# Performance work log

Hardware: AMD Instinct MI355X
Metric: run time of the kernel (lower is better)

Reference implementation:

```python
import jax, jax.numpy as jnp
import numpy as np

N, E, D, L = 50000, 800000, 128, 2
EPS = 1e-10


def mobius_add(x, y, c):
    # c: shape [1], broadcasts against [N,1]
    xy = jnp.sum(x * y, axis=-1, keepdims=True)
    x2 = jnp.sum(x * x, axis=-1, keepdims=True)
    y2 = jnp.sum(y * y, axis=-1, keepdims=True)
    num = (1 + 2 * c * xy + c * y2) * x + (1 - c * x2) * y
    den = 1 + 2 * c * xy + (c ** 2) * x2 * y2
    return num / den


def log_map(x, y, c):
    ym = mobius_add(-x, y, c)
    n = jnp.maximum(jnp.linalg.norm(ym, axis=-1, keepdims=True), EPS)
    sc = jnp.sqrt(c)
    return (2.0 / sc) * jnp.arctanh(sc * n) * ym / n


def exp_map(x, v, c):
    n = jnp.maximum(jnp.linalg.norm(v, axis=-1, keepdims=True), EPS)
    sc = jnp.sqrt(c)
    second = jnp.tanh(sc * n / 2.0) * v / (sc * n)
    return mobius_add(x, second, c)


def l2norm(x):
    return x / jnp.maximum(jnp.linalg.norm(x, axis=-1, keepdims=True), 1e-12)


def mean_agg(h, src, dst, n_nodes):
    # copy_u + mean reduce: mean of h[src] grouped by dst; zero-degree -> 0
    msum = jax.ops.segment_sum(h[src], dst, num_segments=n_nodes)
    deg = jax.ops.segment_sum(jnp.ones((src.shape[0], 1), h.dtype), dst, num_segments=n_nodes)
    return msum / jnp.maximum(deg, 1.0)


def setup_inputs() -> dict:
    key = jax.random.key(0)
    ks = jax.random.split(key, 12)
    scale = 1.0 / np.sqrt(D)
    return {
        "src": jax.random.randint(ks[0], (E,), 0, N, dtype=jnp.int32),
        "dst": jax.random.randint(ks[1], (E,), 0, N, dtype=jnp.int32),
        "e_emb": jax.random.normal(ks[2], (N, D), dtype=jnp.float32),
        "b_emb": 0.01 * jax.random.normal(ks[3], (N, D), dtype=jnp.float32),  # inside Poincare ball
        "s_emb": jax.random.normal(ks[4], (N, D), dtype=jnp.float32),
        "e_W": scale * jax.random.normal(ks[5], (L, D, D), dtype=jnp.float32),
        "e_b": jnp.zeros((L, D), dtype=jnp.float32),
        "b_W": scale * jax.random.normal(ks[6], (L, D, D), dtype=jnp.float32),
        "b_b": jnp.zeros((L, D), dtype=jnp.float32),
        "s_W": scale * jax.random.normal(ks[7], (L, D, D), dtype=jnp.float32),
        "s_b": jnp.zeros((L, D), dtype=jnp.float32),
        "b_curvature": jnp.ones((1,), dtype=jnp.float32),
        "s_curvature": jnp.ones((1,), dtype=jnp.float32),
    }


def reference(src, dst, e_emb, b_emb, s_emb, e_W, e_b, b_W, b_b, s_W, s_b, b_curvature, s_curvature):
    n = e_emb.shape[0]
    origin = jnp.zeros((1, b_emb.shape[-1]), dtype=b_emb.dtype)
    for l in range(L):
        # Euclidean: transform -> mean aggregate -> LeakyReLU(0.2)
        h = e_emb @ e_W[l].T + e_b[l]
        e_emb = mean_agg(h, src, dst, n)
        e_emb = jnp.where(e_emb > 0, e_emb, 0.2 * e_emb)
        # Hyperbolic: log map to tangent -> transform -> mean aggregate -> exp map
        tangent = log_map(origin, b_emb, b_curvature)
        hb = tangent @ b_W[l].T + b_b[l]
        neigh_b = mean_agg(hb, src, dst, n)
        b_emb = exp_map(origin, neigh_b, b_curvature)
        # Spherical: normalize -> transform -> normalize -> mean aggregate -> normalize
        hs = l2norm(l2norm(s_emb) @ s_W[l].T + s_b[l])
        s_emb = l2norm(mean_agg(hs, src, dst, n))
    return (e_emb, b_emb, s_emb)
```

## Files before the change

### kernel.cpp

```cpp
#include <hip/hip_runtime.h>
#include <math.h>

#define DD 128
typedef unsigned int   u32;
typedef unsigned short u16;
typedef short bf16x8 __attribute__((ext_vector_type(8)));
typedef float f32x4  __attribute__((ext_vector_type(4)));

__device__ __forceinline__ float lo2f(u32 p){ return __uint_as_float(p << 16); }
__device__ __forceinline__ float hi2f(u32 p){ return __uint_as_float(p & 0xFFFF0000u); }
__device__ __forceinline__ u16 f2bf(float f){
    u32 u = __float_as_uint(f);
    return (u16)((u + 0x7fffu + ((u >> 16) & 1u)) >> 16);
}

__global__ void k_hist(const int* __restrict__ dst, int* __restrict__ deg, int E){
    int i = blockIdx.x*256 + threadIdx.x;
    if (i < E) atomicAdd(&deg[dst[i]], 1);
}

__global__ void k_chunksum(const int* __restrict__ deg, int* __restrict__ csum,
                           float* __restrict__ invdeg, int n){
    __shared__ int sdata[256];
    int t = threadIdx.x;
    int i0 = blockIdx.x*512 + t*2;
    int a = (i0     < n) ? deg[i0]   : 0;
    int b = (i0 + 1 < n) ? deg[i0+1] : 0;
    if (i0     < n) invdeg[i0]   = 1.0f / (float)max(a, 1);
    if (i0 + 1 < n) invdeg[i0+1] = 1.0f / (float)max(b, 1);
    sdata[t] = a + b; __syncthreads();
    for (int off = 128; off > 0; off >>= 1){
        if (t < off) sdata[t] += sdata[t+off];
        __syncthreads();
    }
    if (t == 0) csum[blockIdx.x] = sdata[0];
}

__global__ void k_scanchunks(int* __restrict__ csum, int nchunks, int* __restrict__ row_ptr, int n){
    if (threadIdx.x == 0){
        int acc = 0;
        for (int i = 0; i < nchunks; i++){ int v = csum[i]; csum[i] = acc; acc += v; }
        row_ptr[n] = acc;
    }
}

__global__ void k_scanwithin(const int* __restrict__ deg, const int* __restrict__ csum,
                             int* __restrict__ row_ptr, int n){
    __shared__ int s[256];
    int t = threadIdx.x;
    int i0 = blockIdx.x*512 + t*2;
    int a = (i0     < n) ? deg[i0]   : 0;
    int b = (i0 + 1 < n) ? deg[i0+1] : 0;
    int tsum = a + b;
    s[t] = tsum; __syncthreads();
    for (int off = 1; off < 256; off <<= 1){
        int v = (t >= off) ? s[t-off] : 0;
        __syncthreads();
        s[t] += v;
        __syncthreads();
    }
    int excl = s[t] - tsum + csum[blockIdx.x];
    if (i0     < n) row_ptr[i0]   = excl;
    if (i0 + 1 < n) row_ptr[i0+1] = excl + a;
}

__global__ void k_fill(const int* __restrict__ src, const int* __restrict__ dst,
                       const int* __restrict__ row_ptr, int* __restrict__ cursor,
                       int* __restrict__ sorted_src, int E){
    int i = blockIdx.x*256 + threadIdx.x;
    if (i < E){
        int d = dst[i];
        int p = atomicAdd(&cursor[d], 1);
        sorted_src[row_ptr[d] + p] = src[i];
    }
}

__global__ void k_w2b(const float* __restrict__ in, u16* __restrict__ out, int n){
    int i = blockIdx.x*256 + threadIdx.x;
    if (i < n) out[i] = f2bf(in[i]);
}

template<int PRE, int POST>
__global__ __launch_bounds__(256, 4)
void k_gemm_mfma(const float* __restrict__ X, const u16* __restrict__ Wb,
                 const float* __restrict__ bias, u16* __restrict__ Y, int n_rows,
                 const float* __restrict__ cptr){
    int t = threadIdx.x;
    int wave = t >> 6, lane = t & 63;
    int q = lane >> 4, m = lane & 15;
    int rowbase = blockIdx.x*64 + wave*16;
    int gr = min(rowbase + m, n_rows - 1);

    float4 xv[8];
    const float4* xp = (const float4*)(X + (size_t)gr*DD);
    #pragma unroll
    for (int c = 0; c < 4; c++){
        xv[2*c]   = xp[c*8 + q*2];
        xv[2*c+1] = xp[c*8 + q*2 + 1];
    }

    float scale = 1.0f;
    if (PRE != 0){
        float ss = 0.f;
        #pragma unroll
        for (int i = 0; i < 8; i++)
            ss += xv[i].x*xv[i].x + xv[i].y*xv[i].y + xv[i].z*xv[i].z + xv[i].w*xv[i].w;
        ss += __shfl_xor(ss, 16, 64);
        ss += __shfl_xor(ss, 32, 64);
        float nrm = sqrtf(ss);
        if (PRE == 1){
            float c  = cptr[0];
            c = (c > 0.f && c < 1e30f) ? c : 1.0f;
            float sc = sqrtf(c);
            float n2 = fmaxf(nrm, 1e-10f);
            float a  = fminf(sc*n2, 0.99999994f);
            scale = (2.0f/sc) * atanhf(a) / n2;
        } else {
            scale = 1.0f / fmaxf(nrm, 1e-12f);
        }
    }

    bf16x8 af[4];
    #pragma unroll
    for (int c = 0; c < 4; c++){
        const float* xf = (const float*)&xv[2*c];
        #pragma unroll
        for (int j = 0; j < 8; j++) af[c][j] = (short)f2bf(xf[j]*scale);
    }

    f32x4 acc[8];
    #pragma unroll
    for (int tl = 0; tl < 8; tl++) acc[tl] = (f32x4){0.f,0.f,0.f,0.f};

    const u16* wb = Wb + (size_t)m*DD + q*8;
    #pragma unroll
    for (int c = 0; c < 4; c++){
        #pragma unroll
        for (int tl = 0; tl < 8; tl++){
            bf16x8 bfr = *(const bf16x8*)(wb + (size_t)tl*16*DD + c*32);
            acc[tl] = __builtin_amdgcn_mfma_f32_16x16x32_bf16(af[c], bfr, acc[tl], 0, 0, 0);
        }
    }

    #pragma unroll
    for (int tl = 0; tl < 8; tl++){
        float bv = bias[tl*16 + m];
        #pragma unroll
        for (int r = 0; r < 4; r++) acc[tl][r] += bv;
    }
    if (POST == 1){
        float ssr[4] = {0.f,0.f,0.f,0.f};
        #pragma unroll
        for (int tl = 0; tl < 8; tl++)
            #pragma unroll
            for (int r = 0; r < 4; r++) ssr[r] += acc[tl][r]*acc[tl][r];
        #pragma unroll
        for (int r = 0; r < 4; r++){
            float s = ssr[r];
            s += __shfl_xor(s, 1, 64);
            s += __shfl_xor(s, 2, 64);
            s += __shfl_xor(s, 4, 64);
            s += __shfl_xor(s, 8, 64);
            float sc = 1.0f / fmaxf(sqrtf(s), 1e-12f);
            #pragma unroll
            for (int tl = 0; tl < 8; tl++) acc[tl][r] *= sc;
        }
    }
    #pragma unroll
    for (int r = 0; r < 4; r++){
        int grow = rowbase + q*4 + r;
        if (grow < n_rows){
            #pragma unroll
            for (int tl = 0; tl < 8; tl++)
                Y[(size_t)grow*DD + tl*16 + m] = f2bf(acc[tl][r]);
        }
    }
}

template<int MODE>
__global__ void k_agg(const u32* __restrict__ h,
                      const int* __restrict__ row_ptr, const int* __restrict__ sorted_src,
                      const float* __restrict__ invdeg,
                      float* __restrict__ outbuf, int n_rows, const float* __restrict__ cptr){
    int wid = (blockIdx.x*256 + threadIdx.x) >> 6;
    if (wid >= n_rows) return;
    int lane = threadIdx.x & 63;
    int beg = row_ptr[wid], end = row_ptr[wid+1];
    float ax = 0.f, ay = 0.f;
    for (int j0 = beg; j0 < end; j0 += 64){
        int cnt = min(64, end - j0);
        int my = (j0 + lane < end) ? sorted_src[j0 + lane] : 0;
        int k = 0;
        for (; k + 8 <= cnt; k += 8){
            u32 p0 = h[(size_t)__shfl(my, k+0, 64)*64 + lane];
            u32 p1 = h[(size_t)__shfl(my, k+1, 64)*64 + lane];
            u32 p2 = h[(size_t)__shfl(my, k+2, 64)*64 + lane];
            u32 p3 = h[(size_t)__shfl(my, k+3, 64)*64 + lane];
            u32 p4 = h[(size_t)__shfl(my, k+4, 64)*64 + lane];
            u32 p5 = h[(size_t)__shfl(my, k+5, 64)*64 + lane];
            u32 p6 = h[(size_t)__shfl(my, k+6, 64)*64 + lane];
            u32 p7 = h[(size_t)__shfl(my, k+7, 64)*64 + lane];
            ax += lo2f(p0); ay += hi2f(p0);
            ax += lo2f(p1); ay += hi2f(p1);
            ax += lo2f(p2); ay += hi2f(p2);
            ax += lo2f(p3); ay += hi2f(p3);
            ax += lo2f(p4); ay += hi2f(p4);
            ax += lo2f(p5); ay += hi2f(p5);
            ax += lo2f(p6); ay += hi2f(p6);
            ax += lo2f(p7); ay += hi2f(p7);
        }
        for (; k < cnt; k++){
            u32 p = h[(size_t)__shfl(my, k, 64)*64 + lane];
            ax += lo2f(p); ay += hi2f(p);
        }
    }
    float inv = invdeg[wid];
    ax *= inv; ay *= inv;
    float ox, oy;
    if (MODE == 0){
        ox = ax > 0.f ? ax : 0.2f*ax;
        oy = ay > 0.f ? ay : 0.2f*ay;
    } else {
        float ss = ax*ax + ay*ay;
        #pragma unroll
        for (int m = 32; m > 0; m >>= 1) ss += __shfl_xor(ss, m, 64);
        float nrm = sqrtf(ss);
        float scale;
        if (MODE == 1){
            float c  = cptr[0];
            c = (c > 0.f && c < 1e30f) ? c : 1.0f;
            float sc = sqrtf(c);
            float n2 = fmaxf(nrm, 1e-10f);
            scale = tanhf(sc*n2*0.5f) / (sc*n2);
        } else {
            scale = 1.0f / fmaxf(nrm, 1e-12f);
        }
        ox = ax*scale; oy = ay*scale;
    }
    *(float2*)(outbuf + (size_t)wid*DD + lane*2) = make_float2(ox, oy);
}

extern "C" void kernel_launch(void* const* d_in, const int* in_sizes, int n_in,
                              void* d_out, int out_size, void* d_ws, size_t ws_size,
                              hipStream_t stream){
    const int*   src = (const int*)d_in[0];
    const int*   dst = (const int*)d_in[1];
    const float* emb_in[3] = {(const float*)d_in[2], (const float*)d_in[3], (const float*)d_in[4]};
    const float* W_in[3]   = {(const float*)d_in[5], (const float*)d_in[7], (const float*)d_in[9]};
    const float* b_in[3]   = {(const float*)d_in[6], (const float*)d_in[8], (const float*)d_in[10]};
    const float* b_c       = (const float*)d_in[11];

    const int E  = in_sizes[0];
    const int ND = in_sizes[2];
    const int N  = ND / DD;
    const int Lnum = in_sizes[5] / (DD*DD);
    const int nw = Lnum*DD*DD;
    const int nchunks = (N + 511) / 512;

    char* w = (char*)d_ws;
    auto alloc = [&](size_t bytes)->char*{
        char* p = w; w += (bytes + 255) & ~(size_t)255; return p;
    };
    u32*   h         = (u32*)  alloc((size_t)ND*2);
    u16*   Wb[3];
    for (int i = 0; i < 3; i++) Wb[i] = (u16*)alloc((size_t)nw*2);
    float* invdeg    = (float*)alloc((size_t)N*4);
    int*   deg       = (int*)  alloc((size_t)N*4);
    int*   row_ptr   = (int*)  alloc((size_t)(N+1)*4);
    int*   cursor    = (int*)  alloc((size_t)N*4);
    int*   csum      = (int*)  alloc((size_t)nchunks*4);
    int*   sorted_src= (int*)  alloc((size_t)E*4);
    (void)ws_size; (void)n_in; (void)out_size;

    float* out_e = (float*)d_out;
    float* out_b = out_e + ND;
    float* out_s = out_e + 2*ND;

    hipMemsetAsync(deg,    0, (size_t)N*4, stream);
    hipMemsetAsync(cursor, 0, (size_t)N*4, stream);

    const int TB = 256;
    for (int i = 0; i < 3; i++)
        k_w2b<<<(nw+TB-1)/TB, TB, 0, stream>>>(W_in[i], Wb[i], nw);

    k_hist<<<(E+TB-1)/TB, TB, 0, stream>>>(dst, deg, E);
    k_chunksum<<<nchunks, 256, 0, stream>>>(deg, csum, invdeg, N);
    k_scanchunks<<<1, 64, 0, stream>>>(csum, nchunks, row_ptr, N);
    k_scanwithin<<<nchunks, 256, 0, stream>>>(deg, csum, row_ptr, N);
    k_fill<<<(E+TB-1)/TB, TB, 0, stream>>>(src, dst, row_ptr, cursor, sorted_src, E);

    const int rowblocks  = (N + 3) / 4;
    const int gemmblocks = (N + 63) / 64;

    const float* se = emb_in[0];
    const float* sb = emb_in[1];
    const float* ss = emb_in[2];

    for (int l = 0; l < Lnum; l++){
        k_gemm_mfma<0,0><<<gemmblocks, 256, 0, stream>>>(se, Wb[0] + (size_t)l*DD*DD,
                                                         b_in[0] + (size_t)l*DD, (u16*)h, N, b_c);
        k_agg<0><<<rowblocks, 256, 0, stream>>>(h, row_ptr, sorted_src, invdeg, out_e, N, b_c);
        se = out_e;
        k_gemm_mfma<1,0><<<gemmblocks, 256, 0, stream>>>(sb, Wb[1] + (size_t)l*DD*DD,
                                                         b_in[1] + (size_t)l*DD, (u16*)h, N, b_c);
        k_agg<1><<<rowblocks, 256, 0, stream>>>(h, row_ptr, sorted_src, invdeg, out_b, N, b_c);
        sb = out_b;
        k_gemm_mfma<2,1><<<gemmblocks, 256, 0, stream>>>(ss, Wb[2] + (size_t)l*DD*DD,
                                                         b_in[2] + (size_t)l*DD, (u16*)h, N, b_c);
        k_agg<2><<<rowblocks, 256, 0, stream>>>(h, row_ptr, sorted_src, invdeg, out_s, N, b_c);
        ss = out_s;
    }
}
```

Measured before the change: 580.1 us.

## Fuse three branch GEMMs and aggregations into single kernels with vectorized gathers

Batches the Euclidean, hyperbolic and spherical GEMMs into one launch using a grid y-dimension, and fuses the three mean aggregations into one kernel that reads the neighbour list once and gathers 16-byte chunks for all three feature buffers. Each wave now handles four edges in parallel with lane groups and reduces across groups via shuffles. The chunk scan is parallelized, and the fill kernel writes cursor positions directly, which removes one memset and the row_ptr lookup. This needs three bf16 intermediate buffers instead of one and increases register pressure in the aggregation kernel.

```diff
diff --git a/kernel.cpp b/kernel.cpp
--- a/kernel.cpp
+++ b/kernel.cpp
@@ -36,16 +36,37 @@
     if (t == 0) csum[blockIdx.x] = sdata[0];
 }
 
-__global__ void k_scanchunks(int* __restrict__ csum, int nchunks, int* __restrict__ row_ptr, int n){
-    if (threadIdx.x == 0){
-        int acc = 0;
-        for (int i = 0; i < nchunks; i++){ int v = csum[i]; csum[i] = acc; acc += v; }
-        row_ptr[n] = acc;
-    }
+__global__ void k_scanchunks(int* __restrict__ csum, int nchunks,
+                             int* __restrict__ row_ptr, int n){
+    __shared__ int s[256];
+    __shared__ int carry_sh;
+    int t = threadIdx.x;
+    if (t == 0) carry_sh = 0;
+    __syncthreads();
+    for (int base = 0; base < nchunks; base += 256){
+        int i = base + t;
+        int v = (i < nchunks) ? csum[i] : 0;
+        s[t] = v;
+        __syncthreads();
+        for (int off = 1; off < 256; off <<= 1){
+            int u = (t >= off) ? s[t-off] : 0;
+            __syncthreads();
+            s[t] += u;
+            __syncthreads();
+        }
+        int carry = carry_sh;
+        int excl  = carry + s[t] - v;
+        if (i < nchunks) csum[i] = excl;
+        int tot = s[255];
+        __syncthreads();
+        if (t == 0) carry_sh = carry + tot;
+        __syncthreads();
+    }
+    if (t == 0) row_ptr[n] = carry_sh;
 }
 
 __global__ void k_scanwithin(const int* __restrict__ deg, const int* __restrict__ csum,
-                             int* __restrict__ row_ptr, int n){
+                             int* __restrict__ row_ptr, int* __restrict__ cursor, int n){
     __shared__ int s[256];
     int t = threadIdx.x;
     int i0 = blockIdx.x*512 + t*2;
@@ -60,31 +81,34 @@
         __syncthreads();
     }
     int excl = s[t] - tsum + csum[blockIdx.x];
-    if (i0     < n) row_ptr[i0]   = excl;
-    if (i0 + 1 < n) row_ptr[i0+1] = excl + a;
+    if (i0     < n){ row_ptr[i0]   = excl;     cursor[i0]   = excl;     }
+    if (i0 + 1 < n){ row_ptr[i0+1] = excl + a; cursor[i0+1] = excl + a; }
 }
 
 __global__ void k_fill(const int* __restrict__ src, const int* __restrict__ dst,
-                       const int* __restrict__ row_ptr, int* __restrict__ cursor,
-                       int* __restrict__ sorted_src, int E){
+                       int* __restrict__ cursor, int* __restrict__ sorted_src, int E){
     int i = blockIdx.x*256 + threadIdx.x;
     if (i < E){
-        int d = dst[i];
-        int p = atomicAdd(&cursor[d], 1);
-        sorted_src[row_ptr[d] + p] = src[i];
-    }
-}
-
-__global__ void k_w2b(const float* __restrict__ in, u16* __restrict__ out, int n){
+        int p = atomicAdd(&cursor[dst[i]], 1);
+        sorted_src[p] = src[i];
+    }
+}
+
+__global__ void k_w2b3(const float* __restrict__ w0, const float* __restrict__ w1,
+                       const float* __restrict__ w2,
+                       u16* __restrict__ o0, u16* __restrict__ o1, u16* __restrict__ o2,
+                       int nw){
     int i = blockIdx.x*256 + threadIdx.x;
-    if (i < n) out[i] = f2bf(in[i]);
+    if (i >= nw) return;
+    const float* s = (blockIdx.y == 0) ? w0 : (blockIdx.y == 1) ? w1 : w2;
+    u16*         o = (blockIdx.y == 0) ? o0 : (blockIdx.y == 1) ? o1 : o2;
+    o[i] = f2bf(s[i]);
 }
 
 template<int PRE, int POST>
-__global__ __launch_bounds__(256, 4)
-void k_gemm_mfma(const float* __restrict__ X, const u16* __restrict__ Wb,
-                 const float* __restrict__ bias, u16* __restrict__ Y, int n_rows,
-                 const float* __restrict__ cptr){
+__device__ __forceinline__ void gemm_body(const float* __restrict__ X, const u16* __restrict__ Wb,
+                                          const float* __restrict__ bias, u16* __restrict__ Y,
+                                          int n_rows, const float* __restrict__ cptr){
     int t = threadIdx.x;
     int wave = t >> 6, lane = t & 63;
     int q = lane >> 4, m = lane & 15;
@@ -177,67 +201,103 @@
     }
 }
 
-template<int MODE>
-__global__ void k_agg(const u32* __restrict__ h,
-                      const int* __restrict__ row_ptr, const int* __restrict__ sorted_src,
-                      const float* __restrict__ invdeg,
-                      float* __restrict__ outbuf, int n_rows, const float* __restrict__ cptr){
+__global__ __launch_bounds__(256, 4)
+void k_gemm3(const float* __restrict__ Xe, const float* __restrict__ Xb, const float* __restrict__ Xs,
+             const u16* __restrict__ We, const u16* __restrict__ Wh, const u16* __restrict__ Ws,
+             const float* __restrict__ be, const float* __restrict__ bb, const float* __restrict__ bs,
+             u16* __restrict__ Ye, u16* __restrict__ Yb, u16* __restrict__ Ys,
+             int n_rows, const float* __restrict__ cptr){
+    if (blockIdx.y == 0)      gemm_body<0,0>(Xe, We, be, Ye, n_rows, cptr);
+    else if (blockIdx.y == 1) gemm_body<1,0>(Xb, Wh, bb, Yb, n_rows, cptr);
+    else                      gemm_body<2,1>(Xs, Ws, bs, Ys, n_rows, cptr);
+}
+
+__device__ __forceinline__ void acc8(float* a, uint4 p){
+    a[0] += lo2f(p.x); a[1] += hi2f(p.x);
+    a[2] += lo2f(p.y); a[3] += hi2f(p.y);
+    a[4] += lo2f(p.z); a[5] += hi2f(p.z);
+    a[6] += lo2f(p.w); a[7] += hi2f(p.w);
+}
+
+__global__ __launch_bounds__(256)
+void k_agg3(const u32* __restrict__ he, const u32* __restrict__ hb, const u32* __restrict__ hs,
+            const int* __restrict__ row_ptr, const int* __restrict__ sorted_src,
+            const float* __restrict__ invdeg,
+            float* __restrict__ out_e, float* __restrict__ out_b, float* __restrict__ out_s,
+            int n_rows, const float* __restrict__ cptr){
     int wid = (blockIdx.x*256 + threadIdx.x) >> 6;
     if (wid >= n_rows) return;
     int lane = threadIdx.x & 63;
+    int g = lane >> 4, c = lane & 15;
     int beg = row_ptr[wid], end = row_ptr[wid+1];
-    float ax = 0.f, ay = 0.f;
-    for (int j0 = beg; j0 < end; j0 += 64){
-        int cnt = min(64, end - j0);
-        int my = (j0 + lane < end) ? sorted_src[j0 + lane] : 0;
-        int k = 0;
-        for (; k + 8 <= cnt; k += 8){
-            u32 p0 = h[(size_t)__shfl(my, k+0, 64)*64 + lane];
-            u32 p1 = h[(size_t)__shfl(my, k+1, 64)*64 + lane];
-            u32 p2 = h[(size_t)__shfl(my, k+2, 64)*64 + lane];
-            u32 p3 = h[(size_t)__shfl(my, k+3, 64)*64 + lane];
-            u32 p4 = h[(size_t)__shfl(my, k+4, 64)*64 + lane];
-            u32 p5 = h[(size_t)__shfl(my, k+5, 64)*64 + lane];
-            u32 p6 = h[(size_t)__shfl(my, k+6, 64)*64 + lane];
-            u32 p7 = h[(size_t)__shfl(my, k+7, 64)*64 + lane];
-            ax += lo2f(p0); ay += hi2f(p0);
-            ax += lo2f(p1); ay += hi2f(p1);
-            ax += lo2f(p2); ay += hi2f(p2);
-            ax += lo2f(p3); ay += hi2f(p3);
-            ax += lo2f(p4); ay += hi2f(p4);
-            ax += lo2f(p5); ay += hi2f(p5);
-            ax += lo2f(p6); ay += hi2f(p6);
-            ax += lo2f(p7); ay += hi2f(p7);
-        }
-        for (; k < cnt; k++){
-            u32 p = h[(size_t)__shfl(my, k, 64)*64 + lane];
-            ax += lo2f(p); ay += hi2f(p);
-        }
+    int coff = c*4;
+
+    float ae[8], ab[8], as_[8];
+    #pragma unroll
+    for (int i = 0; i < 8; i++){ ae[i] = 0.f; ab[i] = 0.f; as_[i] = 0.f; }
+
+    int p = beg + g;
+    for (; p + 4 < end; p += 8){
+        size_t o0 = (size_t)sorted_src[p]  *64 + coff;
+        size_t o1 = (size_t)sorted_src[p+4]*64 + coff;
+        uint4 e0 = *(const uint4*)(he + o0);
+        uint4 b0 = *(const uint4*)(hb + o0);
+        uint4 s0 = *(const uint4*)(hs + o0);
+        uint4 e1 = *(const uint4*)(he + o1);
+        uint4 b1 = *(const uint4*)(hb + o1);
+        uint4 s1 = *(const uint4*)(hs + o1);
+        acc8(ae, e0); acc8(ab, b0); acc8(as_, s0);
+        acc8(ae, e1); acc8(ab, b1); acc8(as_, s1);
+    }
+    if (p < end){
+        size_t o0 = (size_t)sorted_src[p]*64 + coff;
+        uint4 e0 = *(const uint4*)(he + o0);
+        uint4 b0 = *(const uint4*)(hb + o0);
+        uint4 s0 = *(const uint4*)(hs + o0);
+        acc8(ae, e0); acc8(ab, b0); acc8(as_, s0);
+    }
+
+    #pragma unroll
+    for (int i = 0; i < 8; i++){
+        ae[i]  += __shfl_xor(ae[i],  16, 64); ae[i]  += __shfl_xor(ae[i],  32, 64);
+        ab[i]  += __shfl_xor(ab[i],  16, 64); ab[i]  += __shfl_xor(ab[i],  32, 64);
+        as_[i] += __shfl_xor(as_[i], 16, 64); as_[i] += __shfl_xor(as_[i], 32, 64);
     }
     float inv = invdeg[wid];
-    ax *= inv; ay *= inv;
-    float ox, oy;
-    if (MODE == 0){
-        ox = ax > 0.f ? ax : 0.2f*ax;
-        oy = ay > 0.f ? ay : 0.2f*ay;
-    } else {
-        float ss = ax*ax + ay*ay;
-        #pragma unroll
-        for (int m = 32; m > 0; m >>= 1) ss += __shfl_xor(ss, m, 64);
-        float nrm = sqrtf(ss);
-        float scale;
-        if (MODE == 1){
-            float c  = cptr[0];
-            c = (c > 0.f && c < 1e30f) ? c : 1.0f;
-            float sc = sqrtf(c);
-            float n2 = fmaxf(nrm, 1e-10f);
-            scale = tanhf(sc*n2*0.5f) / (sc*n2);
-        } else {
-            scale = 1.0f / fmaxf(nrm, 1e-12f);
-        }
-        ox = ax*scale; oy = ay*scale;
-    }
-    *(float2*)(outbuf + (size_t)wid*DD + lane*2) = make_float2(ox, oy);
+    #pragma unroll
+    for (int i = 0; i < 8; i++){ ae[i] *= inv; ab[i] *= inv; as_[i] *= inv; }
+
+    float ssb = 0.f, sss = 0.f;
+    #pragma unroll
+    for (int i = 0; i < 8; i++){ ssb += ab[i]*ab[i]; sss += as_[i]*as_[i]; }
+    #pragma unroll
+    for (int msk = 1; msk < 16; msk <<= 1){
+        ssb += __shfl_xor(ssb, msk, 64);
+        sss += __shfl_xor(sss, msk, 64);
+    }
+
+    if (g == 0){
+        float o[8];
+        #pragma unroll
+        for (int i = 0; i < 8; i++) o[i] = ae[i] > 0.f ? ae[i] : 0.2f*ae[i];
+        float4* dstp = (float4*)(out_e + (size_t)wid*DD + c*8);
+        dstp[0] = make_float4(o[0],o[1],o[2],o[3]);
+        dstp[1] = make_float4(o[4],o[5],o[6],o[7]);
+    } else if (g == 1){
+        float cc = cptr[0];
+        cc = (cc > 0.f && cc < 1e30f) ? cc : 1.0f;
+        float sc = sqrtf(cc);
+        float n2 = fmaxf(sqrtf(ssb), 1e-10f);
+        float scale = tanhf(sc*n2*0.5f) / (sc*n2);
+        float4* dstp = (float4*)(out_b + (size_t)wid*DD + c*8);
+        dstp[0] = make_float4(ab[0]*scale, ab[1]*scale, ab[2]*scale, ab[3]*scale);
+        dstp[1] = make_float4(ab[4]*scale, ab[5]*scale, ab[6]*scale, ab[7]*scale);
+    } else if (g == 2){
+        float scale = 1.0f / fmaxf(sqrtf(sss), 1e-12f);
+        float4* dstp = (float4*)(out_s + (size_t)wid*DD + c*8);
+        dstp[0] = make_float4(as_[0]*scale, as_[1]*scale, as_[2]*scale, as_[3]*scale);
+        dstp[1] = make_float4(as_[4]*scale, as_[5]*scale, as_[6]*scale, as_[7]*scale);
+    }
 }
 
 extern "C" void kernel_launch(void* const* d_in, const int* in_sizes, int n_in,
@@ -261,7 +321,9 @@
     auto alloc = [&](size_t bytes)->char*{
         char* p = w; w += (bytes + 255) & ~(size_t)255; return p;
     };
-    u32*   h         = (u32*)  alloc((size_t)ND*2);
+    u32*   hE        = (u32*)  alloc((size_t)ND*2);
+    u32*   hB        = (u32*)  alloc((size_t)ND*2);
+    u32*   hS        = (u32*)  alloc((size_t)ND*2);
     u16*   Wb[3];
     for (int i = 0; i < 3; i++) Wb[i] = (u16*)alloc((size_t)nw*2);
     float* invdeg    = (float*)alloc((size_t)N*4);
@@ -276,18 +338,16 @@
     float* out_b = out_e + ND;
     float* out_s = out_e + 2*ND;
 
-    hipMemsetAsync(deg,    0, (size_t)N*4, stream);
-    hipMemsetAsync(cursor, 0, (size_t)N*4, stream);
+    hipMemsetAsync(deg, 0, (size_t)N*4, stream);
 
     const int TB = 256;
-    for (int i = 0; i < 3; i++)
-        k_w2b<<<(nw+TB-1)/TB, TB, 0, stream>>>(W_in[i], Wb[i], nw);
-
+    k_w2b3<<<dim3((nw+TB-1)/TB, 3), TB, 0, stream>>>(W_in[0], W_in[1], W_in[2],
+                                                     Wb[0], Wb[1], Wb[2], nw);
     k_hist<<<(E+TB-1)/TB, TB, 0, stream>>>(dst, deg, E);
     k_chunksum<<<nchunks, 256, 0, stream>>>(deg, csum, invdeg, N);
-    k_scanchunks<<<1, 64, 0, stream>>>(csum, nchunks, row_ptr, N);
-    k_scanwithin<<<nchunks, 256, 0, stream>>>(deg, csum, row_ptr, N);
-    k_fill<<<(E+TB-1)/TB, TB, 0, stream>>>(src, dst, row_ptr, cursor, sorted_src, E);
+    k_scanchunks<<<1, 256, 0, stream>>>(csum, nchunks, row_ptr, N);
+    k_scanwithin<<<nchunks, 256, 0, stream>>>(deg, csum, row_ptr, cursor, N);
+    k_fill<<<(E+TB-1)/TB, TB, 0, stream>>>(src, dst, cursor, sorted_src, E);
 
     const int rowblocks  = (N + 3) / 4;
     const int gemmblocks = (N + 63) / 64;
@@ -297,17 +357,13 @@
     const float* ss = emb_in[2];
 
     for (int l = 0; l < Lnum; l++){
-        k_gemm_mfma<0,0><<<gemmblocks, 256, 0, stream>>>(se, Wb[0] + (size_t)l*DD*DD,
-                                                         b_in[0] + (size_t)l*DD, (u16*)h, N, b_c);
-        k_agg<0><<<rowblocks, 256, 0, stream>>>(h, row_ptr, sorted_src, invdeg, out_e, N, b_c);
-        se = out_e;
-        k_gemm_mfma<1,0><<<gemmblocks, 256, 0, stream>>>(sb, Wb[1] + (size_t)l*DD*DD,
-                                                         b_in[1] + (size_t)l*DD, (u16*)h, N, b_c);
-        k_agg<1><<<rowblocks, 256, 0, stream>>>(h, row_ptr, sorted_src, invdeg, out_b, N, b_c);
-        sb = out_b;
-        k_gemm_mfma<2,1><<<gemmblocks, 256, 0, stream>>>(ss, Wb[2] + (size_t)l*DD*DD,
-                                                         b_in[2] + (size_t)l*DD, (u16*)h, N, b_c);
-        k_agg<2><<<rowblocks, 256, 0, stream>>>(h, row_ptr, sorted_src, invdeg, out_s, N, b_c);
-        ss = out_s;
-    }
-}
+        k_gemm3<<<dim3(gemmblocks, 3), 256, 0, stream>>>(
+            se, sb, ss,
+            Wb[0] + (size_t)l*DD*DD, Wb[1] + (size_t)l*DD*DD, Wb[2] + (size_t)l*DD*DD,
+            b_in[0] + (size_t)l*DD,  b_in[1] + (size_t)l*DD,  b_in[2] + (size_t)l*DD,
+            (u16*)hE, (u16*)hB, (u16*)hS, N, b_c);
+        k_agg3<<<rowblocks, 256, 0, stream>>>(hE, hB, hS, row_ptr, sorted_src, invdeg,
+                                              out_e, out_b, out_s, N, b_c);
+        se = out_e; sb = out_b; ss = out_s;
+    }
+}
```

New measurement: 512.5 us. 11.7% less time.
